# Performance work log

Measured on AMD Instinct MI355X. Metric: run time of the kernel, lower is better.

Reference implementation:

```python
import jax, jax.numpy as jnp
import numpy as np

E = 100000  # entity count
TEMP = 0.8
EPS = 1e-5


def _layer_norm(x, g, b):
    m = jnp.mean(x, axis=-1, keepdims=True)
    v = jnp.mean((x - m) ** 2, axis=-1, keepdims=True)
    return (x - m) / jnp.sqrt(v + EPS) * g + b


def setup_inputs() -> dict:
    key = jax.random.key(0)
    ks = jax.random.split(key, 20)
    f32 = jnp.float32
    inp = {
        "utype_mask": jnp.zeros((E,), dtype=bool),
        "entity_mask": jax.random.bernoulli(ks[0], 0.5, (E,)),
        "entity_encodings": jax.random.normal(ks[1], (E, 256), dtype=f32),
        "autoregressive_encoding": jax.random.normal(ks[2], (1024,), dtype=f32),
        "self_unit_ct": 150000,
        # Conv1d(256, 32, 1) == pointwise linear
        "Wk": jax.random.normal(ks[3], (32, 256), dtype=f32) * 0.05,
        "bk": jax.random.normal(ks[4], (32,), dtype=f32) * 0.05,
        # argenc[0]: Linear(1024, 256)
        "W0": jax.random.normal(ks[5], (256, 1024), dtype=f32) * 0.05,
        "b0": jax.random.normal(ks[6], (256,), dtype=f32) * 0.05,
        # argenc[1]: ReLU -> Linear(256, 32) -> ReLU
        "W1": jax.random.normal(ks[7], (32, 256), dtype=f32) * 0.05,
        "b1": jax.random.normal(ks[8], (32,), dtype=f32) * 0.05,
        # LSTM(64, 32) gates
        "Wf": jax.random.normal(ks[9], (32, 64), dtype=f32) * 0.05,
        "bf": jax.random.normal(ks[10], (32,), dtype=f32) * 0.05,
        "Wi0": jax.random.normal(ks[11], (32, 64), dtype=f32) * 0.05,
        "bi0": jax.random.normal(ks[12], (32,), dtype=f32) * 0.05,
        "Wi1": jax.random.normal(ks[13], (32, 64), dtype=f32) * 0.05,
        "bi1": jax.random.normal(ks[14], (32,), dtype=f32) * 0.05,
        "Wo": jax.random.normal(ks[15], (32, 64), dtype=f32) * 0.05,
        "bo": jax.random.normal(ks[16], (32,), dtype=f32) * 0.05,
        # shared LayerNorm(32) params
        "ln_g": jnp.ones((32,), dtype=f32),
        "ln_b": jnp.zeros((32,), dtype=f32),
    }
    return inp


def reference(utype_mask, entity_mask, entity_encodings, autoregressive_encoding,
              self_unit_ct, Wk, bk, W0, b0, W1, b1, Wf, bf, Wi0, bi0, Wi1, bi1,
              Wo, bo, ln_g, ln_b):
    ect = entity_encodings.shape[0]
    em = (~entity_mask).astype(jnp.float32)  # logical_not * 1.0
    # entity keys: Conv1d(256,32,1) pointwise -> [32, E]
    keys = entity_encodings @ Wk.T + bk  # [E, 32]

    # static condition (self_unit_ct and ect are Python ints / static shapes)
    assert self_unit_ct - ect > 0, "branch must be taken (matches original code path)"

    intermed = autoregressive_encoding @ W0.T + b0          # Linear(1024,256)
    intermed = jax.nn.relu(intermed)
    intermed = jax.nn.relu(intermed @ W1.T + b1)            # Linear(256,32)
    x = jnp.concatenate([intermed, jnp.zeros((32,), intermed.dtype)])  # [64]

    # LSTM cell with prev_hidden = 0
    forget = _layer_norm(jax.nn.sigmoid(x @ Wf.T + bf), ln_g, ln_b)
    _ = forget  # forget * 0 == 0
    remember = _layer_norm(jax.nn.sigmoid(x @ Wi0.T + bi0) * jnp.tanh(x @ Wi1.T + bi1), ln_g, ln_b)
    new_h = remember
    query = jnp.tanh(new_h) * _layer_norm(jax.nn.sigmoid(x @ Wo.T + bo), ln_g, ln_b)  # [32]

    similarity = (query[None, :] @ keys.T)  # [1, E]
    logit = jax.nn.sigmoid(similarity)
    # temp_softmax: exp(log(l)/T), nan_to_num, normalize if sum != 0
    vec = jnp.nan_to_num(jnp.exp(jnp.log(logit) / TEMP))
    s = jnp.sum(vec)
    unit_logits = jnp.where(s != 0, vec / jnp.where(s != 0, s, 1.0), vec)  # [1, E]

    # multinomial(1, p).argmax == categorical sample (deterministic key stands in for np RNG)
    pick = jax.random.categorical(jax.random.key(42), jnp.log(unit_logits.squeeze()))
    valid = em[pick] != 0
    targeted_unit = jnp.zeros((ect,), jnp.float32).at[pick].set(jnp.where(valid, 1.0, 0.0))
    return unit_logits, targeted_unit
```

## Files before the change

kernel.cpp:

```cpp
#include <hip/hip_runtime.h>
#include <cstdint>
#include <float.h>
#include <math.h>


__device__ __forceinline__ float sigmoidf_(float x) { return 1.0f / (1.0f + expf(-x)); }

__global__ __launch_bounds__(256) void head1_kernel(
    const float* __restrict__ aue, const float* __restrict__ W0,
    const float* __restrict__ b0, float* __restrict__ inter_out)
{
    __shared__ __align__(16) float a_s[1024];
    const int t = threadIdx.x;
    for (int k = t; k < 1024; k += 256) a_s[k] = aue[k];
    __syncthreads();

    const int wave = t >> 6, lane = t & 63;
    const int row = blockIdx.x * 4 + wave;
    const float* wr = W0 + row * 1024;
    float acc = 0.0f;
    #pragma unroll
    for (int p = 0; p < 4; ++p) {
        int k = p * 256 + lane * 4;
        float4 w = *reinterpret_cast<const float4*>(wr + k);
        acc += w.x * a_s[k] + w.y * a_s[k+1] + w.z * a_s[k+2] + w.w * a_s[k+3];
    }
    #pragma unroll
    for (int off = 32; off; off >>= 1) acc += __shfl_xor(acc, off);
    if (lane == 0) {
        float v = acc + b0[row];
        inter_out[row] = v > 0.0f ? v : 0.0f;
    }
}

__global__ __launch_bounds__(256) void head2_kernel(
    const float* __restrict__ inter, const float* __restrict__ Wk, const float* __restrict__ bk,
    const float* __restrict__ W1, const float* __restrict__ b1,
    const float* __restrict__ Wi0, const float* __restrict__ bi0,
    const float* __restrict__ Wi1, const float* __restrict__ bi1,
    const float* __restrict__ Wo, const float* __restrict__ bo,
    const float* __restrict__ ln_g, const float* __restrict__ ln_b,
    float* __restrict__ q256_out, float* __restrict__ c_out)
{
    __shared__ __align__(16) float inter_s[256];
    __shared__ float x_s[64];
    __shared__ float tmp_s[64];
    __shared__ float stat_s[4];
    const int t = threadIdx.x;
    inter_s[t] = inter[t];
    __syncthreads();

    const int wave = t >> 6, lane = t & 63;
    for (int r = wave; r < 32; r += 4) {
        const float* wr = W1 + r * 256;
        int k = lane * 4;
        float4 w = *reinterpret_cast<const float4*>(wr + k);
        float acc = w.x * inter_s[k] + w.y * inter_s[k+1] + w.z * inter_s[k+2] + w.w * inter_s[k+3];
        #pragma unroll
        for (int off = 32; off; off >>= 1) acc += __shfl_xor(acc, off);
        if (lane == 0) {
            float v = acc + b1[r];
            x_s[r] = v > 0.0f ? v : 0.0f;
        }
    }
    if (t < 32) x_s[32 + t] = 0.0f;
    __syncthreads();

    if (t < 96) {
        const int g = t >> 5, r = t & 31;
        const float* W = (g == 0) ? Wi0 : (g == 1) ? Wi1 : Wo;
        const float* B = (g == 0) ? bi0 : (g == 1) ? bi1 : bo;
        float acc = B[r];
        const float* wr = W + r * 64;
        for (int k = 0; k < 64; ++k) acc += wr[k] * x_s[k];
        if (g == 0)      tmp_s[r] = sigmoidf_(acc);
        else if (g == 1) x_s[32 + r] = tanhf(acc);
        else             tmp_s[32 + r] = sigmoidf_(acc);
    }
    __syncthreads();
    if (t < 32) tmp_s[t] = tmp_s[t] * x_s[32 + t];
    __syncthreads();

    if (t == 0) {
        float m1 = 0.0f, m2 = 0.0f;
        for (int k = 0; k < 32; ++k) { m1 += tmp_s[k]; m2 += tmp_s[32 + k]; }
        m1 *= (1.0f / 32.0f); m2 *= (1.0f / 32.0f);
        float v1 = 0.0f, v2 = 0.0f;
        for (int k = 0; k < 32; ++k) {
            float d1 = tmp_s[k] - m1;      v1 += d1 * d1;
            float d2 = tmp_s[32 + k] - m2; v2 += d2 * d2;
        }
        stat_s[0] = m1; stat_s[1] = 1.0f / sqrtf(v1 * (1.0f / 32.0f) + 1e-5f);
        stat_s[2] = m2; stat_s[3] = 1.0f / sqrtf(v2 * (1.0f / 32.0f) + 1e-5f);
    }
    __syncthreads();

    if (t < 32) {
        float rem = (tmp_s[t]      - stat_s[0]) * stat_s[1] * ln_g[t] + ln_b[t];
        float og  = (tmp_s[32 + t] - stat_s[2]) * stat_s[3] * ln_g[t] + ln_b[t];
        x_s[t] = tanhf(rem) * og;
    }
    __syncthreads();

    float q = 0.0f;
    for (int j = 0; j < 32; ++j) q += x_s[j] * Wk[j * 256 + t];
    q256_out[t] = q;
    if (t == 0) {
        float c = 0.0f;
        for (int j = 0; j < 32; ++j) c += x_s[j] * bk[j];
        c_out[0] = c;
    }
}

__global__ __launch_bounds__(256) void vec_kernel(
    const float* __restrict__ enc, const float* __restrict__ q256,
    const float* __restrict__ c_in, float* __restrict__ out_vec,
    float* __restrict__ partials, int E)
{
    __shared__ __align__(16) float q_s[256];
    __shared__ float wsum_s[4];
    const int t = threadIdx.x;
    q_s[t] = q256[t];
    __syncthreads();
    const float c = c_in[0];
    const int wave = t >> 6, lane = t & 63;
    const int gwave = blockIdx.x * 4 + wave;
    const int nwave = gridDim.x * 4;
    const float4 qv = *reinterpret_cast<const float4*>(q_s + lane * 4);
    float lsum = 0.0f;

    int i = gwave;
    for (; i + nwave < E; i += 2 * nwave) {
        const float4 e0 = *reinterpret_cast<const float4*>(enc + (size_t)i * 256 + lane * 4);
        const float4 e1 = *reinterpret_cast<const float4*>(enc + (size_t)(i + nwave) * 256 + lane * 4);
        float d0 = e0.x * qv.x + e0.y * qv.y + e0.z * qv.z + e0.w * qv.w;
        float d1 = e1.x * qv.x + e1.y * qv.y + e1.z * qv.z + e1.w * qv.w;
        #pragma unroll
        for (int off = 32; off; off >>= 1) {
            d0 += __shfl_xor(d0, off);
            d1 += __shfl_xor(d1, off);
        }
        if (lane == 0) {
            float v0 = expf(logf(1.0f / (1.0f + expf(-(d0 + c)))) / 0.8f);
            float v1 = expf(logf(1.0f / (1.0f + expf(-(d1 + c)))) / 0.8f);
            out_vec[i] = v0;
            out_vec[i + nwave] = v1;
            lsum += v0;
            lsum += v1;
        }
    }
    if (i < E) {
        const float4 e = *reinterpret_cast<const float4*>(enc + (size_t)i * 256 + lane * 4);
        float d = e.x * qv.x + e.y * qv.y + e.z * qv.z + e.w * qv.w;
        #pragma unroll
        for (int off = 32; off; off >>= 1) d += __shfl_xor(d, off);
        if (lane == 0) {
            float v = expf(logf(1.0f / (1.0f + expf(-(d + c)))) / 0.8f);
            out_vec[i] = v;
            lsum += v;
        }
    }

    if (lane == 0) wsum_s[wave] = lsum;
    __syncthreads();
    if (t == 0) partials[blockIdx.x] = (wsum_s[0] + wsum_s[1]) + (wsum_s[2] + wsum_s[3]);
}

__device__ __forceinline__ uint32_t rotl_(uint32_t x, int r) { return (x << r) | (x >> (32 - r)); }

__device__ __forceinline__ void threefry_0_42(uint32_t c0, uint32_t c1,
                                              uint32_t& o0, uint32_t& o1)
{
    const uint32_t ks0 = 0u, ks1 = 42u;
    const uint32_t ks2 = 0x1BD11BDAu ^ ks0 ^ ks1;
    uint32_t x0 = c0 + ks0, x1 = c1 + ks1;
#define TF_R(r) { x0 += x1; x1 = rotl_(x1, r); x1 ^= x0; }
    TF_R(13) TF_R(15) TF_R(26) TF_R(6)
    x0 += ks1; x1 += ks2 + 1u;
    TF_R(17) TF_R(29) TF_R(16) TF_R(24)
    x0 += ks2; x1 += ks0 + 2u;
    TF_R(13) TF_R(15) TF_R(26) TF_R(6)
    x0 += ks0; x1 += ks1 + 3u;
    TF_R(17) TF_R(29) TF_R(16) TF_R(24)
    x0 += ks1; x1 += ks2 + 4u;
    TF_R(13) TF_R(15) TF_R(26) TF_R(6)
    x0 += ks2; x1 += ks0 + 5u;
#undef TF_R
    o0 = x0; o1 = x1;
}

__global__ __launch_bounds__(256) void gumbel_argmax_kernel(
    float* __restrict__ dout, const float* __restrict__ partials, int NBP,
    double* __restrict__ amax_s, int* __restrict__ amax_i, int E)
{
    const int t = threadIdx.x;
    const int i = blockIdx.x * 256 + t;

    __shared__ float red[256];
    {
        float a = 0.0f;
        for (int k = t; k < NBP; k += 256) a += partials[k];
        red[t] = a;
        __syncthreads();
        for (int off = 128; off; off >>= 1) {
            if (t < off) red[t] += red[t + off];
            __syncthreads();
        }
    }
    const float s = red[0];

    double best = -INFINITY;
    int bidx = 0x7FFFFFFF;
    if (i < E) {
        float v = dout[i];
        float p32 = (s != 0.0f) ? (v / s) : v;
        dout[i] = p32;
        dout[E + i] = 0.0f;

        uint32_t hi, lo;
        threefry_0_42((uint32_t)i, (uint32_t)(i + E), hi, lo);
        uint64_t bits = ((uint64_t)hi << 32) | (uint64_t)lo;
        uint64_t fb = (bits >> 12) | 0x3FF0000000000000ull;
        double f = __longlong_as_double((long long)fb);
        const double tiny = 2.2250738585072014e-308;
        double u = fmax(tiny, (f - 1.0) + tiny);
        double g = -log(-log(u));
        best = log((double)v) + g;
        bidx = i;
    }
    __shared__ double s_s[256];
    __shared__ int    s_i[256];
    s_s[t] = best; s_i[t] = bidx;
    __syncthreads();
    for (int off = 128; off; off >>= 1) {
        if (t < off) {
            double o = s_s[t + off]; int oi = s_i[t + off];
            if (o > s_s[t] || (o == s_s[t] && oi < s_i[t])) { s_s[t] = o; s_i[t] = oi; }
        }
        __syncthreads();
    }
    if (t == 0) { amax_s[blockIdx.x] = s_s[0]; amax_i[blockIdx.x] = s_i[0]; }
}

__global__ __launch_bounds__(256) void pick_kernel(
    const double* __restrict__ amax_s, const int* __restrict__ amax_i, int nb,
    const void* __restrict__ emask_raw, float* __restrict__ dout, int E)
{
    __shared__ double s_s[256];
    __shared__ int    s_i[256];
    const int t = threadIdx.x;
    double best = -INFINITY; int bidx = 0x7FFFFFFF;
    for (int k = t; k < nb; k += 256) {
        double sc = amax_s[k]; int i = amax_i[k];
        if (sc > best || (sc == best && i < bidx)) { best = sc; bidx = i; }
    }
    s_s[t] = best; s_i[t] = bidx;
    __syncthreads();
    for (int off = 128; off; off >>= 1) {
        if (t < off) {
            double o = s_s[t + off]; int oi = s_i[t + off];
            if (o > s_s[t] || (o == s_s[t] && oi < s_i[t])) { s_s[t] = o; s_i[t] = oi; }
        }
        __syncthreads();
    }
    if (t == 0) {
        int pick = s_i[0];
        const uint32_t* as_u32 = (const uint32_t*)emask_raw;
        bool int_layout = true;
        for (int k = 0; k < 64; ++k) {
            if (as_u32[k] > 1u) { int_layout = false; break; }
        }
        int mval = int_layout ? (int)as_u32[pick]
                              : (int)((const unsigned char*)emask_raw)[pick];
        dout[E + pick] = (mval == 0) ? 1.0f : 0.0f;
    }
}

extern "C" void kernel_launch(void* const* d_in, const int* in_sizes, int n_in,
                              void* d_out, int out_size, void* d_ws, size_t ws_size,
                              hipStream_t stream)
{
    (void)n_in; (void)out_size; (void)ws_size;
    const void*  emask = d_in[1];
    const float* enc   = (const float*)d_in[2];
    const float* aue   = (const float*)d_in[3];
    const float* Wk    = (const float*)d_in[5];
    const float* bk    = (const float*)d_in[6];
    const float* W0    = (const float*)d_in[7];
    const float* b0    = (const float*)d_in[8];
    const float* W1    = (const float*)d_in[9];
    const float* b1    = (const float*)d_in[10];
    const float* Wi0   = (const float*)d_in[13];
    const float* bi0   = (const float*)d_in[14];
    const float* Wi1   = (const float*)d_in[15];
    const float* bi1   = (const float*)d_in[16];
    const float* Wo    = (const float*)d_in[17];
    const float* bo    = (const float*)d_in[18];
    const float* ln_g  = (const float*)d_in[19];
    const float* ln_b  = (const float*)d_in[20];

    const int E = in_sizes[1];
    float* out = (float*)d_out;
    float* ws  = (float*)d_ws;
    float*  q256     = ws;
    float*  cval     = ws + 256;
    float*  partials = ws + 512;
    double* amax_s   = (double*)(ws + 4608);
    int*    amax_i   = (int*)(ws + 6912);
    float*  inter    = ws + 7424;

    const int NB2 = 2048;
    const int NB4 = (E + 255) / 256;

    head1_kernel<<<64, 256, 0, stream>>>(aue, W0, b0, inter);
    head2_kernel<<<1, 256, 0, stream>>>(inter, Wk, bk, W1, b1,
                                        Wi0, bi0, Wi1, bi1, Wo, bo, ln_g, ln_b,
                                        q256, cval);
    vec_kernel<<<NB2, 256, 0, stream>>>(enc, q256, cval, out, partials, E);
    gumbel_argmax_kernel<<<NB4, 256, 0, stream>>>(out, partials, NB2, amax_s, amax_i, E);
    pick_kernel<<<1, 256, 0, stream>>>(amax_s, amax_i, NB4, emask, out, E);
}
```

Before: 50.33 us.

## Fuse Gumbel argmax into similarity kernel and merge pick into finalize

Computes the Gumbel-max sampling score inside the vec kernel as v / -log(u), which ranks the same as log v + Gumbel noise, and keeps a running per-block argmax there. The separate pick kernel goes away. The finalize kernel now normalises the output, writes the one-hot vector and reduces the per-block argmax candidates itself. This saves one kernel launch and one full pass of threefry and log work in its own kernel. In exchange, every finalize block redundantly reduces all 2048 candidates, and lane 0 of each wave does the double-precision RNG and log work inside the memory-bound loop.

```diff
diff --git a/kernel.cpp b/kernel.cpp
--- a/kernel.cpp
+++ b/kernel.cpp
@@ -5,166 +5,6 @@
 
 
 __device__ __forceinline__ float sigmoidf_(float x) { return 1.0f / (1.0f + expf(-x)); }
-
-__global__ __launch_bounds__(256) void head1_kernel(
-    const float* __restrict__ aue, const float* __restrict__ W0,
-    const float* __restrict__ b0, float* __restrict__ inter_out)
-{
-    __shared__ __align__(16) float a_s[1024];
-    const int t = threadIdx.x;
-    for (int k = t; k < 1024; k += 256) a_s[k] = aue[k];
-    __syncthreads();
-
-    const int wave = t >> 6, lane = t & 63;
-    const int row = blockIdx.x * 4 + wave;
-    const float* wr = W0 + row * 1024;
-    float acc = 0.0f;
-    #pragma unroll
-    for (int p = 0; p < 4; ++p) {
-        int k = p * 256 + lane * 4;
-        float4 w = *reinterpret_cast<const float4*>(wr + k);
-        acc += w.x * a_s[k] + w.y * a_s[k+1] + w.z * a_s[k+2] + w.w * a_s[k+3];
-    }
-    #pragma unroll
-    for (int off = 32; off; off >>= 1) acc += __shfl_xor(acc, off);
-    if (lane == 0) {
-        float v = acc + b0[row];
-        inter_out[row] = v > 0.0f ? v : 0.0f;
-    }
-}
-
-__global__ __launch_bounds__(256) void head2_kernel(
-    const float* __restrict__ inter, const float* __restrict__ Wk, const float* __restrict__ bk,
-    const float* __restrict__ W1, const float* __restrict__ b1,
-    const float* __restrict__ Wi0, const float* __restrict__ bi0,
-    const float* __restrict__ Wi1, const float* __restrict__ bi1,
-    const float* __restrict__ Wo, const float* __restrict__ bo,
-    const float* __restrict__ ln_g, const float* __restrict__ ln_b,
-    float* __restrict__ q256_out, float* __restrict__ c_out)
-{
-    __shared__ __align__(16) float inter_s[256];
-    __shared__ float x_s[64];
-    __shared__ float tmp_s[64];
-    __shared__ float stat_s[4];
-    const int t = threadIdx.x;
-    inter_s[t] = inter[t];
-    __syncthreads();
-
-    const int wave = t >> 6, lane = t & 63;
-    for (int r = wave; r < 32; r += 4) {
-        const float* wr = W1 + r * 256;
-        int k = lane * 4;
-        float4 w = *reinterpret_cast<const float4*>(wr + k);
-        float acc = w.x * inter_s[k] + w.y * inter_s[k+1] + w.z * inter_s[k+2] + w.w * inter_s[k+3];
-        #pragma unroll
-        for (int off = 32; off; off >>= 1) acc += __shfl_xor(acc, off);
-        if (lane == 0) {
-            float v = acc + b1[r];
-            x_s[r] = v > 0.0f ? v : 0.0f;
-        }
-    }
-    if (t < 32) x_s[32 + t] = 0.0f;
-    __syncthreads();
-
-    if (t < 96) {
-        const int g = t >> 5, r = t & 31;
-        const float* W = (g == 0) ? Wi0 : (g == 1) ? Wi1 : Wo;
-        const float* B = (g == 0) ? bi0 : (g == 1) ? bi1 : bo;
-        float acc = B[r];
-        const float* wr = W + r * 64;
-        for (int k = 0; k < 64; ++k) acc += wr[k] * x_s[k];
-        if (g == 0)      tmp_s[r] = sigmoidf_(acc);
-        else if (g == 1) x_s[32 + r] = tanhf(acc);
-        else             tmp_s[32 + r] = sigmoidf_(acc);
-    }
-    __syncthreads();
-    if (t < 32) tmp_s[t] = tmp_s[t] * x_s[32 + t];
-    __syncthreads();
-
-    if (t == 0) {
-        float m1 = 0.0f, m2 = 0.0f;
-        for (int k = 0; k < 32; ++k) { m1 += tmp_s[k]; m2 += tmp_s[32 + k]; }
-        m1 *= (1.0f / 32.0f); m2 *= (1.0f / 32.0f);
-        float v1 = 0.0f, v2 = 0.0f;
-        for (int k = 0; k < 32; ++k) {
-            float d1 = tmp_s[k] - m1;      v1 += d1 * d1;
-            float d2 = tmp_s[32 + k] - m2; v2 += d2 * d2;
-        }
-        stat_s[0] = m1; stat_s[1] = 1.0f / sqrtf(v1 * (1.0f / 32.0f) + 1e-5f);
-        stat_s[2] = m2; stat_s[3] = 1.0f / sqrtf(v2 * (1.0f / 32.0f) + 1e-5f);
-    }
-    __syncthreads();
-
-    if (t < 32) {
-        float rem = (tmp_s[t]      - stat_s[0]) * stat_s[1] * ln_g[t] + ln_b[t];
-        float og  = (tmp_s[32 + t] - stat_s[2]) * stat_s[3] * ln_g[t] + ln_b[t];
-        x_s[t] = tanhf(rem) * og;
-    }
-    __syncthreads();
-
-    float q = 0.0f;
-    for (int j = 0; j < 32; ++j) q += x_s[j] * Wk[j * 256 + t];
-    q256_out[t] = q;
-    if (t == 0) {
-        float c = 0.0f;
-        for (int j = 0; j < 32; ++j) c += x_s[j] * bk[j];
-        c_out[0] = c;
-    }
-}
-
-__global__ __launch_bounds__(256) void vec_kernel(
-    const float* __restrict__ enc, const float* __restrict__ q256,
-    const float* __restrict__ c_in, float* __restrict__ out_vec,
-    float* __restrict__ partials, int E)
-{
-    __shared__ __align__(16) float q_s[256];
-    __shared__ float wsum_s[4];
-    const int t = threadIdx.x;
-    q_s[t] = q256[t];
-    __syncthreads();
-    const float c = c_in[0];
-    const int wave = t >> 6, lane = t & 63;
-    const int gwave = blockIdx.x * 4 + wave;
-    const int nwave = gridDim.x * 4;
-    const float4 qv = *reinterpret_cast<const float4*>(q_s + lane * 4);
-    float lsum = 0.0f;
-
-    int i = gwave;
-    for (; i + nwave < E; i += 2 * nwave) {
-        const float4 e0 = *reinterpret_cast<const float4*>(enc + (size_t)i * 256 + lane * 4);
-        const float4 e1 = *reinterpret_cast<const float4*>(enc + (size_t)(i + nwave) * 256 + lane * 4);
-        float d0 = e0.x * qv.x + e0.y * qv.y + e0.z * qv.z + e0.w * qv.w;
-        float d1 = e1.x * qv.x + e1.y * qv.y + e1.z * qv.z + e1.w * qv.w;
-        #pragma unroll
-        for (int off = 32; off; off >>= 1) {
-            d0 += __shfl_xor(d0, off);
-            d1 += __shfl_xor(d1, off);
-        }
-        if (lane == 0) {
-            float v0 = expf(logf(1.0f / (1.0f + expf(-(d0 + c)))) / 0.8f);
-            float v1 = expf(logf(1.0f / (1.0f + expf(-(d1 + c)))) / 0.8f);
-            out_vec[i] = v0;
-            out_vec[i + nwave] = v1;
-            lsum += v0;
-            lsum += v1;
-        }
-    }
-    if (i < E) {
-        const float4 e = *reinterpret_cast<const float4*>(enc + (size_t)i * 256 + lane * 4);
-        float d = e.x * qv.x + e.y * qv.y + e.z * qv.z + e.w * qv.w;
-        #pragma unroll
-        for (int off = 32; off; off >>= 1) d += __shfl_xor(d, off);
-        if (lane == 0) {
-            float v = expf(logf(1.0f / (1.0f + expf(-(d + c)))) / 0.8f);
-            out_vec[i] = v;
-            lsum += v;
-        }
-    }
-
-    if (lane == 0) wsum_s[wave] = lsum;
-    __syncthreads();
-    if (t == 0) partials[blockIdx.x] = (wsum_s[0] + wsum_s[1]) + (wsum_s[2] + wsum_s[3]);
-}
 
 __device__ __forceinline__ uint32_t rotl_(uint32_t x, int r) { return (x << r) | (x >> (32 - r)); }
 
@@ -189,9 +29,207 @@
     o0 = x0; o1 = x1;
 }
 
-__global__ __launch_bounds__(256) void gumbel_argmax_kernel(
+__device__ __forceinline__ double gumbel_score(float v, int i, int E)
+{
+    uint32_t hi, lo;
+    threefry_0_42((uint32_t)i, (uint32_t)(i + E), hi, lo);
+    uint64_t bits = ((uint64_t)hi << 32) | (uint64_t)lo;
+    uint64_t fb = (bits >> 12) | 0x3FF0000000000000ull;
+    double f = __longlong_as_double((long long)fb);
+    const double tiny = 2.2250738585072014e-308;
+    double u = fmax(tiny, (f - 1.0) + tiny);
+    return (double)v / (-log(u));
+}
+
+__global__ __launch_bounds__(256) void head1_kernel(
+    const float* __restrict__ aue, const float* __restrict__ W0,
+    const float* __restrict__ b0, float* __restrict__ inter_out)
+{
+    __shared__ __align__(16) float a_s[1024];
+    const int t = threadIdx.x;
+    for (int k = t; k < 1024; k += 256) a_s[k] = aue[k];
+    __syncthreads();
+
+    const int wave = t >> 6, lane = t & 63;
+    const int row = blockIdx.x * 4 + wave;
+    const float* wr = W0 + row * 1024;
+    float acc = 0.0f;
+    #pragma unroll
+    for (int p = 0; p < 4; ++p) {
+        int k = p * 256 + lane * 4;
+        float4 w = *reinterpret_cast<const float4*>(wr + k);
+        acc += w.x * a_s[k] + w.y * a_s[k+1] + w.z * a_s[k+2] + w.w * a_s[k+3];
+    }
+    #pragma unroll
+    for (int off = 32; off; off >>= 1) acc += __shfl_xor(acc, off);
+    if (lane == 0) {
+        float v = acc + b0[row];
+        inter_out[row] = v > 0.0f ? v : 0.0f;
+    }
+}
+
+__global__ __launch_bounds__(256) void head2_kernel(
+    const float* __restrict__ inter, const float* __restrict__ Wk, const float* __restrict__ bk,
+    const float* __restrict__ W1, const float* __restrict__ b1,
+    const float* __restrict__ Wi0, const float* __restrict__ bi0,
+    const float* __restrict__ Wi1, const float* __restrict__ bi1,
+    const float* __restrict__ Wo, const float* __restrict__ bo,
+    const float* __restrict__ ln_g, const float* __restrict__ ln_b,
+    float* __restrict__ q256_out, float* __restrict__ c_out)
+{
+    __shared__ __align__(16) float inter_s[256];
+    __shared__ float x_s[64];
+    __shared__ float tmp_s[64];
+    __shared__ float stat_s[4];
+    const int t = threadIdx.x;
+    inter_s[t] = inter[t];
+    __syncthreads();
+
+    const int wave = t >> 6, lane = t & 63;
+    for (int r = wave; r < 32; r += 4) {
+        const float* wr = W1 + r * 256;
+        int k = lane * 4;
+        float4 w = *reinterpret_cast<const float4*>(wr + k);
+        float acc = w.x * inter_s[k] + w.y * inter_s[k+1] + w.z * inter_s[k+2] + w.w * inter_s[k+3];
+        #pragma unroll
+        for (int off = 32; off; off >>= 1) acc += __shfl_xor(acc, off);
+        if (lane == 0) {
+            float v = acc + b1[r];
+            x_s[r] = v > 0.0f ? v : 0.0f;
+        }
+    }
+    if (t < 32) x_s[32 + t] = 0.0f;
+    __syncthreads();
+
+    if (t < 96) {
+        const int g = t >> 5, r = t & 31;
+        const float* W = (g == 0) ? Wi0 : (g == 1) ? Wi1 : Wo;
+        const float* B = (g == 0) ? bi0 : (g == 1) ? bi1 : bo;
+        float acc = B[r];
+        const float* wr = W + r * 64;
+        for (int k = 0; k < 64; ++k) acc += wr[k] * x_s[k];
+        if (g == 0)      tmp_s[r] = sigmoidf_(acc);
+        else if (g == 1) x_s[32 + r] = tanhf(acc);
+        else             tmp_s[32 + r] = sigmoidf_(acc);
+    }
+    __syncthreads();
+    if (t < 32) tmp_s[t] = tmp_s[t] * x_s[32 + t];
+    __syncthreads();
+
+    if (t == 0) {
+        float m1 = 0.0f, m2 = 0.0f;
+        for (int k = 0; k < 32; ++k) { m1 += tmp_s[k]; m2 += tmp_s[32 + k]; }
+        m1 *= (1.0f / 32.0f); m2 *= (1.0f / 32.0f);
+        float v1 = 0.0f, v2 = 0.0f;
+        for (int k = 0; k < 32; ++k) {
+            float d1 = tmp_s[k] - m1;      v1 += d1 * d1;
+            float d2 = tmp_s[32 + k] - m2; v2 += d2 * d2;
+        }
+        stat_s[0] = m1; stat_s[1] = 1.0f / sqrtf(v1 * (1.0f / 32.0f) + 1e-5f);
+        stat_s[2] = m2; stat_s[3] = 1.0f / sqrtf(v2 * (1.0f / 32.0f) + 1e-5f);
+    }
+    __syncthreads();
+
+    if (t < 32) {
+        float rem = (tmp_s[t]      - stat_s[0]) * stat_s[1] * ln_g[t] + ln_b[t];
+        float og  = (tmp_s[32 + t] - stat_s[2]) * stat_s[3] * ln_g[t] + ln_b[t];
+        x_s[t] = tanhf(rem) * og;
+    }
+    __syncthreads();
+
+    float q = 0.0f;
+    for (int j = 0; j < 32; ++j) q += x_s[j] * Wk[j * 256 + t];
+    q256_out[t] = q;
+    if (t == 0) {
+        float c = 0.0f;
+        for (int j = 0; j < 32; ++j) c += x_s[j] * bk[j];
+        c_out[0] = c;
+    }
+}
+
+__global__ __launch_bounds__(256) void vec_kernel(
+    const float* __restrict__ enc, const float* __restrict__ q256,
+    const float* __restrict__ c_in, float* __restrict__ out_vec,
+    float* __restrict__ partials, double* __restrict__ amax_s,
+    int* __restrict__ amax_i, int E)
+{
+    __shared__ __align__(16) float q_s[256];
+    __shared__ float wsum_s[4];
+    __shared__ double wamax_s[4];
+    __shared__ int    wamax_i[4];
+    const int t = threadIdx.x;
+    q_s[t] = q256[t];
+    __syncthreads();
+    const float c = c_in[0];
+    const int wave = t >> 6, lane = t & 63;
+    const int gwave = blockIdx.x * 4 + wave;
+    const int nwave = gridDim.x * 4;
+    const float4 qv = *reinterpret_cast<const float4*>(q_s + lane * 4);
+    float lsum = 0.0f;
+    double best = -INFINITY;
+    int bidx = 0x7FFFFFFF;
+
+    int i = gwave;
+    for (; i + nwave < E; i += 2 * nwave) {
+        const float4 e0 = *reinterpret_cast<const float4*>(enc + (size_t)i * 256 + lane * 4);
+        const float4 e1 = *reinterpret_cast<const float4*>(enc + (size_t)(i + nwave) * 256 + lane * 4);
+        float d0 = e0.x * qv.x + e0.y * qv.y + e0.z * qv.z + e0.w * qv.w;
+        float d1 = e1.x * qv.x + e1.y * qv.y + e1.z * qv.z + e1.w * qv.w;
+        #pragma unroll
+        for (int off = 32; off; off >>= 1) {
+            d0 += __shfl_xor(d0, off);
+            d1 += __shfl_xor(d1, off);
+        }
+        if (lane == 0) {
+            float v0 = expf(logf(1.0f / (1.0f + expf(-(d0 + c)))) / 0.8f);
+            float v1 = expf(logf(1.0f / (1.0f + expf(-(d1 + c)))) / 0.8f);
+            out_vec[i] = v0;
+            out_vec[i + nwave] = v1;
+            lsum += v0;
+            lsum += v1;
+            double sc0 = gumbel_score(v0, i, E);
+            if (sc0 > best) { best = sc0; bidx = i; }
+            double sc1 = gumbel_score(v1, i + nwave, E);
+            if (sc1 > best) { best = sc1; bidx = i + nwave; }
+        }
+    }
+    if (i < E) {
+        const float4 e = *reinterpret_cast<const float4*>(enc + (size_t)i * 256 + lane * 4);
+        float d = e.x * qv.x + e.y * qv.y + e.z * qv.z + e.w * qv.w;
+        #pragma unroll
+        for (int off = 32; off; off >>= 1) d += __shfl_xor(d, off);
+        if (lane == 0) {
+            float v = expf(logf(1.0f / (1.0f + expf(-(d + c)))) / 0.8f);
+            out_vec[i] = v;
+            lsum += v;
+            double sc = gumbel_score(v, i, E);
+            if (sc > best) { best = sc; bidx = i; }
+        }
+    }
+
+    if (lane == 0) {
+        wsum_s[wave] = lsum;
+        wamax_s[wave] = best;
+        wamax_i[wave] = bidx;
+    }
+    __syncthreads();
+    if (t == 0) {
+        partials[blockIdx.x] = (wsum_s[0] + wsum_s[1]) + (wsum_s[2] + wsum_s[3]);
+        double bb = wamax_s[0]; int bi = wamax_i[0];
+        #pragma unroll
+        for (int w = 1; w < 4; ++w) {
+            double o = wamax_s[w]; int oi = wamax_i[w];
+            if (o > bb || (o == bb && oi < bi)) { bb = o; bi = oi; }
+        }
+        amax_s[blockIdx.x] = bb;
+        amax_i[blockIdx.x] = bi;
+    }
+}
+
+__global__ __launch_bounds__(256) void finalize_kernel(
     float* __restrict__ dout, const float* __restrict__ partials, int NBP,
-    double* __restrict__ amax_s, int* __restrict__ amax_i, int E)
+    const double* __restrict__ amax_s, const int* __restrict__ amax_i,
+    const void* __restrict__ emask_raw, int E)
 {
     const int t = threadIdx.x;
     const int i = blockIdx.x * 256 + t;
@@ -209,70 +247,41 @@
     }
     const float s = red[0];
 
-    double best = -INFINITY;
-    int bidx = 0x7FFFFFFF;
+    __shared__ double s_s[256];
+    __shared__ int    s_i[256];
+    {
+        double best = -INFINITY; int bidx = 0x7FFFFFFF;
+        for (int k = t; k < NBP; k += 256) {
+            double sc = amax_s[k]; int ii = amax_i[k];
+            if (sc > best || (sc == best && ii < bidx)) { best = sc; bidx = ii; }
+        }
+        s_s[t] = best; s_i[t] = bidx;
+        __syncthreads();
+        for (int off = 128; off; off >>= 1) {
+            if (t < off) {
+                double o = s_s[t + off]; int oi = s_i[t + off];
+                if (o > s_s[t] || (o == s_s[t] && oi < s_i[t])) { s_s[t] = o; s_i[t] = oi; }
+            }
+            __syncthreads();
+        }
+    }
+    const int pick = s_i[0];
+
     if (i < E) {
         float v = dout[i];
-        float p32 = (s != 0.0f) ? (v / s) : v;
-        dout[i] = p32;
-        dout[E + i] = 0.0f;
-
-        uint32_t hi, lo;
-        threefry_0_42((uint32_t)i, (uint32_t)(i + E), hi, lo);
-        uint64_t bits = ((uint64_t)hi << 32) | (uint64_t)lo;
-        uint64_t fb = (bits >> 12) | 0x3FF0000000000000ull;
-        double f = __longlong_as_double((long long)fb);
-        const double tiny = 2.2250738585072014e-308;
-        double u = fmax(tiny, (f - 1.0) + tiny);
-        double g = -log(-log(u));
-        best = log((double)v) + g;
-        bidx = i;
-    }
-    __shared__ double s_s[256];
-    __shared__ int    s_i[256];
-    s_s[t] = best; s_i[t] = bidx;
-    __syncthreads();
-    for (int off = 128; off; off >>= 1) {
-        if (t < off) {
-            double o = s_s[t + off]; int oi = s_i[t + off];
-            if (o > s_s[t] || (o == s_s[t] && oi < s_i[t])) { s_s[t] = o; s_i[t] = oi; }
-        }
-        __syncthreads();
-    }
-    if (t == 0) { amax_s[blockIdx.x] = s_s[0]; amax_i[blockIdx.x] = s_i[0]; }
-}
-
-__global__ __launch_bounds__(256) void pick_kernel(
-    const double* __restrict__ amax_s, const int* __restrict__ amax_i, int nb,
-    const void* __restrict__ emask_raw, float* __restrict__ dout, int E)
-{
-    __shared__ double s_s[256];
-    __shared__ int    s_i[256];
-    const int t = threadIdx.x;
-    double best = -INFINITY; int bidx = 0x7FFFFFFF;
-    for (int k = t; k < nb; k += 256) {
-        double sc = amax_s[k]; int i = amax_i[k];
-        if (sc > best || (sc == best && i < bidx)) { best = sc; bidx = i; }
-    }
-    s_s[t] = best; s_i[t] = bidx;
-    __syncthreads();
-    for (int off = 128; off; off >>= 1) {
-        if (t < off) {
-            double o = s_s[t + off]; int oi = s_i[t + off];
-            if (o > s_s[t] || (o == s_s[t] && oi < s_i[t])) { s_s[t] = o; s_i[t] = oi; }
-        }
-        __syncthreads();
-    }
-    if (t == 0) {
-        int pick = s_i[0];
-        const uint32_t* as_u32 = (const uint32_t*)emask_raw;
-        bool int_layout = true;
-        for (int k = 0; k < 64; ++k) {
-            if (as_u32[k] > 1u) { int_layout = false; break; }
-        }
-        int mval = int_layout ? (int)as_u32[pick]
-                              : (int)((const unsigned char*)emask_raw)[pick];
-        dout[E + pick] = (mval == 0) ? 1.0f : 0.0f;
+        dout[i] = (s != 0.0f) ? (v / s) : v;
+        float tu = 0.0f;
+        if (i == pick) {
+            const uint32_t* as_u32 = (const uint32_t*)emask_raw;
+            bool int_layout = true;
+            for (int k = 0; k < 64; ++k) {
+                if (as_u32[k] > 1u) { int_layout = false; break; }
+            }
+            int mval = int_layout ? (int)as_u32[pick]
+                                  : (int)((const unsigned char*)emask_raw)[pick];
+            tu = (mval == 0) ? 1.0f : 0.0f;
+        }
+        dout[E + i] = tu;
     }
 }
 
@@ -304,19 +313,20 @@
     float* ws  = (float*)d_ws;
     float*  q256     = ws;
     float*  cval     = ws + 256;
-    float*  partials = ws + 512;
-    double* amax_s   = (double*)(ws + 4608);
-    int*    amax_i   = (int*)(ws + 6912);
-    float*  inter    = ws + 7424;
+    float*  inter    = ws + 512;
+    float*  partials = ws + 1024;
+    double* amax_s   = (double*)(ws + 4096);
+    int*    amax_i   = (int*)(ws + 8192);
 
     const int NB2 = 2048;
-    const int NB4 = (E + 255) / 256;
+    const int NBF = (E + 255) / 256;
 
     head1_kernel<<<64, 256, 0, stream>>>(aue, W0, b0, inter);
     head2_kernel<<<1, 256, 0, stream>>>(inter, Wk, bk, W1, b1,
                                         Wi0, bi0, Wi1, bi1, Wo, bo, ln_g, ln_b,
                                         q256, cval);
-    vec_kernel<<<NB2, 256, 0, stream>>>(enc, q256, cval, out, partials, E);
-    gumbel_argmax_kernel<<<NB4, 256, 0, stream>>>(out, partials, NB2, amax_s, amax_i, E);
-    pick_kernel<<<1, 256, 0, stream>>>(amax_s, amax_i, NB4, emask, out, E);
-}
+    vec_kernel<<<NB2, 256, 0, stream>>>(enc, q256, cval, out, partials,
+                                        amax_s, amax_i, E);
+    finalize_kernel<<<NBF, 256, 0, stream>>>(out, partials, NB2,
+                                             amax_s, amax_i, emask, E);
+}
```

Measured after the change: 74.55 us. 48.1% more time.
